# Performance work log

Measured on AMD Instinct MI355X. Metric: run time of the kernel, lower is better.

The kernel has to match this reference:

```python
import jax, jax.numpy as jnp
import numpy as np

N_NODES = 50000
N_EDGES = 600000
IN_DIM = 128
OUT_DIM = 128
N_REL = 32
N_BASES = 4
BN_EPS = 1e-5


def setup_inputs() -> dict:
    key = jax.random.key(0)
    ks = jax.random.split(key, 8)
    entity_emb = jax.random.normal(ks[0], (N_NODES, IN_DIM), dtype=jnp.float32)
    bases = jax.random.normal(ks[1], (N_BASES, IN_DIM, OUT_DIM), dtype=jnp.float32) * 0.05
    coefficients = jax.random.normal(ks[2], (N_REL, N_BASES), dtype=jnp.float32) * 0.5
    W_loop = jax.random.normal(ks[3], (IN_DIM, OUT_DIM), dtype=jnp.float32) * 0.05
    b_loop = jnp.zeros((OUT_DIM,), dtype=jnp.float32)
    gamma = jnp.ones((OUT_DIM,), dtype=jnp.float32)
    beta = jnp.zeros((OUT_DIM,), dtype=jnp.float32)
    edge_index = jax.random.randint(ks[4], (2, N_EDGES), 0, N_NODES, dtype=jnp.int32)
    edge_type = jax.random.randint(ks[5], (N_EDGES,), 0, N_REL, dtype=jnp.int32)
    return {"entity_emb": entity_emb, "bases": bases, "coefficients": coefficients,
            "W_loop": W_loop, "b_loop": b_loop, "gamma": gamma, "beta": beta,
            "edge_index": edge_index, "edge_type": edge_type}


def reference(entity_emb, bases, coefficients, W_loop, b_loop, gamma, beta, edge_index, edge_type):
    N = entity_emb.shape[0]
    # self-loop linear
    out = entity_emb @ W_loop + b_loop  # [N, out_dim]
    # basis decomposition: per-relation weight W[r] = sum_b coeff[r,b] * bases[b]
    W = jnp.einsum('rb,bio->rio', coefficients, bases)  # [R, in, out]
    src, dst = edge_index[0], edge_index[1]
    # per-edge message: entity_emb[src_e] @ W[edge_type_e]  (vectorizes the per-relation loop)
    msg = jnp.einsum('ei,eio->eo', entity_emb[src], W[edge_type])  # [E, out]
    out = out + jax.ops.segment_sum(msg, dst, num_segments=N)
    # degree normalization (in-degree over all edges, clamped at 1)
    deg = jax.ops.segment_sum(jnp.ones_like(dst, dtype=out.dtype), dst, num_segments=N)
    out = out / jnp.maximum(deg, 1.0)[:, None]
    # BatchNorm1d (training mode: biased batch stats over node dim)
    mean = jnp.mean(out, axis=0)
    var = jnp.mean((out - mean) ** 2, axis=0)
    out = (out - mean) / jnp.sqrt(var + BN_EPS) * gamma + beta
    return jax.nn.relu(out)
```

## Files before the change

### kernel.cpp

```cpp
#include <hip/hip_runtime.h>
#include <cstdint>

#define NN 50000
#define NE 600000

typedef unsigned short ushort_t;
typedef __bf16 bf16_t;
typedef __attribute__((ext_vector_type(8))) bf16_t bf16x8;
typedef __attribute__((ext_vector_type(8))) ushort_t ushort8;
typedef __attribute__((ext_vector_type(4))) float f32x4;

#define WT_OFF   0ul
#define XG_OFF   40960ul
#define XBF_OFF  16040960ul
#define CNT_OFF  19240960ul
#define CUR_OFF  19290960ul
#define BSUM_OFF 19340960ul
#define BSCN_OFF 19341088ul
#define CS_OFF   19341216ul
#define CSQ_OFF  19341344ul

__device__ __forceinline__ float2 bf2_to_f2(uint32_t u) {
    float2 r;
    r.x = __uint_as_float(u << 16);
    r.y = __uint_as_float(u & 0xffff0000u);
    return r;
}

__device__ __forceinline__ ushort_t f2bf(float f) {
    uint32_t u = __float_as_uint(f);
    u = (u + 0x7fffu + ((u >> 16) & 1u)) >> 16;
    return (ushort_t)u;
}

__device__ __forceinline__ uint32_t f2bf2(float x, float y) {
    return (uint32_t)f2bf(x) | ((uint32_t)f2bf(y) << 16);
}

__device__ __forceinline__ void async_copy16(const void* g, void* l) {
    __builtin_amdgcn_global_load_lds(
        (const __attribute__((address_space(1))) void*)g,
        (__attribute__((address_space(3))) void*)l, 16, 0, 0);
}

__global__ __launch_bounds__(256) void k_prep(
    const float* __restrict__ Wl, const float* __restrict__ bases,
    ushort_t* __restrict__ WT)
{
    const int i = blockIdx.x * 256 + threadIdx.x;
    if (i >= 128 * 640) return;
    const int n = i / 640;
    const int kk = i - n * 640;
    float v;
    if (kk < 128) v = Wl[kk * 128 + n];
    else {
        const int j = kk - 128;
        v = bases[(size_t)(j >> 7) * 16384 + (j & 127) * 128 + n];
    }
    WT[i] = f2bf(v);
}

__global__ __launch_bounds__(256) void k_cast(
    const float* __restrict__ X, ushort_t* __restrict__ Xbf,
    ushort_t* __restrict__ XG)
{
    __shared__ ushort_t L[16][136];
    const int tid = threadIdx.x;
    const int tile = blockIdx.x;
    {
        const int row = tid >> 4, gc = tid & 15;
        const int node = tile * 16 + row;
        const float4* p = (const float4*)(X + (size_t)node * 128 + gc * 8);
        const float4 a = p[0], b = p[1];
        ushort_t t8[8] = { f2bf(a.x), f2bf(a.y), f2bf(a.z), f2bf(a.w),
                           f2bf(b.x), f2bf(b.y), f2bf(b.z), f2bf(b.w) };
        const uint4 v = *(const uint4*)t8;
        *(uint4*)&L[row][gc * 8] = v;
        *(uint4*)(Xbf + (size_t)node * 128 + gc * 8) = v;
    }
    __syncthreads();
    {
        const int g = tid >> 4, r2 = tid & 15;
        const uint4 u = *(const uint4*)&L[r2][g * 8];
        *(uint4*)(XG + (size_t)tile * 10240 + g * 128 + r2 * 8) = u;
    }
}

__global__ __launch_bounds__(256) void k_hist(
    const int* __restrict__ eidx, int* __restrict__ cnt)
{
    const int* __restrict__ dst = eidx + NE;
    for (int e = blockIdx.x * 256 + threadIdx.x; e < NE; e += gridDim.x * 256)
        atomicAdd(cnt + dst[e], 1);
}

__global__ __launch_bounds__(256) void k_scan1(
    const int* __restrict__ cnt, int* __restrict__ curs, int* __restrict__ bsum)
{
    __shared__ int sh[256];
    const int tid = threadIdx.x;
    const int i0 = blockIdx.x * 512 + tid * 2;
    const int v0 = (i0 < NN) ? cnt[i0] : 0;
    const int v1 = (i0 + 1 < NN) ? cnt[i0 + 1] : 0;
    int s = v0 + v1;
    sh[tid] = s;
    __syncthreads();
#pragma unroll
    for (int off = 1; off < 256; off <<= 1) {
        int t = (tid >= off) ? sh[tid - off] : 0;
        __syncthreads();
        sh[tid] += t;
        __syncthreads();
    }
    const int excl = sh[tid] - s;
    if (i0 < NN) curs[i0] = excl;
    if (i0 + 1 < NN) curs[i0 + 1] = excl + v0;
    if (tid == 255) bsum[blockIdx.x] = sh[255];
}

__global__ __launch_bounds__(128) void k_scan2(
    const int* __restrict__ bsum, int* __restrict__ bscan, int nblk)
{
    __shared__ int sh[128];
    const int tid = threadIdx.x;
    int v = (tid < nblk) ? bsum[tid] : 0;
    sh[tid] = v;
    __syncthreads();
#pragma unroll
    for (int off = 1; off < 128; off <<= 1) {
        int t = (tid >= off) ? sh[tid - off] : 0;
        __syncthreads();
        sh[tid] += t;
        __syncthreads();
    }
    if (tid < nblk) bscan[tid] = sh[tid] - v;
}

__global__ __launch_bounds__(256) void k_scan3(
    int* __restrict__ curs, const int* __restrict__ bscan)
{
    const int add = bscan[blockIdx.x];
    const int i0 = blockIdx.x * 512 + threadIdx.x * 2;
    if (i0 < NN) curs[i0] += add;
    if (i0 + 1 < NN) curs[i0 + 1] += add;
}

__global__ __launch_bounds__(256) void k_scatter(
    const int* __restrict__ eidx, const int* __restrict__ etype,
    int* __restrict__ curs, uint32_t* __restrict__ epack)
{
    const int* __restrict__ src = eidx;
    const int* __restrict__ dst = eidx + NE;
    for (int e = blockIdx.x * 256 + threadIdx.x; e < NE; e += gridDim.x * 256) {
        const int d = dst[e];
        const int pos = atomicAdd(curs + d, 1);
        epack[pos] = (uint32_t)src[e] | ((uint32_t)etype[e] << 16);
    }
}

__device__ __forceinline__ void edge_accum8(
    uint32_t ep, const ushort_t* __restrict__ Xbf,
    const float* __restrict__ coeff, int k, float* m)
{
    const int s = ep & 0xffff;
    const int t = ep >> 16;
    const float4 cw = *(const float4*)(coeff + t * 4);
    const uint4 xv = *(const uint4*)(Xbf + (size_t)s * 128 + k * 8);
    float x[8];
    float2 p;
    p = bf2_to_f2(xv.x); x[0] = p.x; x[1] = p.y;
    p = bf2_to_f2(xv.y); x[2] = p.x; x[3] = p.y;
    p = bf2_to_f2(xv.z); x[4] = p.x; x[5] = p.y;
    p = bf2_to_f2(xv.w); x[6] = p.x; x[7] = p.y;
#pragma unroll
    for (int c = 0; c < 8; ++c) {
        m[0 * 8 + c] += cw.x * x[c];
        m[1 * 8 + c] += cw.y * x[c];
        m[2 * 8 + c] += cw.z * x[c];
        m[3 * 8 + c] += cw.w * x[c];
    }
}

__global__ __launch_bounds__(256) void k_gather(
    const ushort_t* __restrict__ Xbf, const uint32_t* __restrict__ epack,
    const int* __restrict__ cnt, const int* __restrict__ curs,
    const float* __restrict__ coeff, ushort_t* __restrict__ XG)
{
    const int lane = threadIdx.x & 63;
    const int w = threadIdx.x >> 6;
    const int sub = lane >> 4;
    const int k = lane & 15;
    const int tile = blockIdx.x;
    const int d = tile * 16 + w * 4 + sub;

    const int n = cnt[d];
    const int end = curs[d];
    int j = end - n;

    float m[32];
#pragma unroll
    for (int i = 0; i < 32; ++i) m[i] = 0.f;

    for (; j + 3 < end; j += 4) {
        const uint32_t e0 = epack[j];
        const uint32_t e1 = epack[j + 1];
        const uint32_t e2 = epack[j + 2];
        const uint32_t e3 = epack[j + 3];
        edge_accum8(e0, Xbf, coeff, k, m);
        edge_accum8(e1, Xbf, coeff, k, m);
        edge_accum8(e2, Xbf, coeff, k, m);
        edge_accum8(e3, Xbf, coeff, k, m);
    }
    for (; j < end; ++j) edge_accum8(epack[j], Xbf, coeff, k, m);

    uint32_t* gb = (uint32_t*)(XG + (size_t)tile * 10240);
#pragma unroll
    for (int b = 0; b < 4; ++b) {
        uint4 v;
        v.x = f2bf2(m[b * 8 + 0], m[b * 8 + 1]);
        v.y = f2bf2(m[b * 8 + 2], m[b * 8 + 3]);
        v.z = f2bf2(m[b * 8 + 4], m[b * 8 + 5]);
        v.w = f2bf2(m[b * 8 + 6], m[b * 8 + 7]);
        *(uint4*)(gb + (16 + b * 16 + k) * 64 + (w * 4 + sub) * 4) = v;
    }
}

__global__ __launch_bounds__(256) void k_gemm_f(
    const ushort_t* __restrict__ XG, const ushort_t* __restrict__ WT,
    const float* __restrict__ bl, const int* __restrict__ cnt,
    float* __restrict__ out, float* __restrict__ colsum,
    float* __restrict__ colsq)
{
    __shared__ ushort_t As[2][10240];
    const int tid = threadIdx.x;
    const int lane = tid & 63;
    const int w = tid >> 6;
    const int row0 = blockIdx.x * 32;
    const int tile0 = blockIdx.x * 2;

#pragma unroll
    for (int k = 0; k < 10; ++k) {
        const int s = w * 10 + k;
        const int tl = s >= 20 ? 1 : 0;
        const int off = s - tl * 20;
        const ushort_t* src = XG + (size_t)(tile0 + tl) * 10240 + off * 512 + lane * 8;
        async_copy16(src, &As[tl][off * 512]);
    }
    __syncthreads();

    const int m = lane & 15;
    const int quad = lane >> 4;
    const ushort_t* bp0 = WT + (size_t)(w * 32 + m) * 640 + quad * 8;
    const ushort_t* bp1 = bp0 + 16 * 640;

    f32x4 cc[2][2];
#pragma unroll
    for (int rt = 0; rt < 2; ++rt)
#pragma unroll
        for (int ct = 0; ct < 2; ++ct)
#pragma unroll
            for (int i = 0; i < 4; ++i) cc[rt][ct][i] = 0.f;

#pragma unroll
    for (int c = 0; c < 20; ++c) {
        const bf16x8 b0 = __builtin_bit_cast(bf16x8, *(const ushort8*)(bp0 + c * 32));
        const bf16x8 b1 = __builtin_bit_cast(bf16x8, *(const ushort8*)(bp1 + c * 32));
        const int aoff = (c * 4 + quad) * 128 + m * 8;
        const bf16x8 a0 = __builtin_bit_cast(bf16x8, *(const ushort8*)&As[0][aoff]);
        const bf16x8 a1 = __builtin_bit_cast(bf16x8, *(const ushort8*)&As[1][aoff]);
        cc[0][0] = __builtin_amdgcn_mfma_f32_16x16x32_bf16(a0, b0, cc[0][0], 0, 0, 0);
        cc[0][1] = __builtin_amdgcn_mfma_f32_16x16x32_bf16(a0, b1, cc[0][1], 0, 0, 0);
        cc[1][0] = __builtin_amdgcn_mfma_f32_16x16x32_bf16(a1, b0, cc[1][0], 0, 0, 0);
        cc[1][1] = __builtin_amdgcn_mfma_f32_16x16x32_bf16(a1, b1, cc[1][1], 0, 0, 0);
    }

    const float blv0 = bl[w * 32 + m];
    const float blv1 = bl[w * 32 + 16 + m];
    float s0 = 0.f, q0 = 0.f, s1 = 0.f, q1 = 0.f;

#pragma unroll
    for (int rt = 0; rt < 2; ++rt) {
        const int rowb = row0 + rt * 16 + quad * 4;
#pragma unroll
        for (int r = 0; r < 4; ++r) {
            const int row = rowb + r;
            if (row < NN) {
                const int dg = cnt[row];
                const float inv = 1.0f / (float)((dg > 0) ? dg : 1);
                float* po = out + (size_t)row * 128 + w * 32 + m;
                const float v0 = (cc[rt][0][r] + blv0) * inv;
                const float v1 = (cc[rt][1][r] + blv1) * inv;
                po[0]  = v0;
                po[16] = v1;
                s0 += v0; q0 += v0 * v0;
                s1 += v1; q1 += v1 * v1;
            }
        }
    }

    s0 += __shfl_down(s0, 32); q0 += __shfl_down(q0, 32);
    s0 += __shfl_down(s0, 16); q0 += __shfl_down(q0, 16);
    s1 += __shfl_down(s1, 32); q1 += __shfl_down(q1, 32);
    s1 += __shfl_down(s1, 16); q1 += __shfl_down(q1, 16);
    if (lane < 16) {
        atomicAdd(colsum + w * 32 + lane, s0);
        atomicAdd(colsq  + w * 32 + lane, q0);
        atomicAdd(colsum + w * 32 + 16 + lane, s1);
        atomicAdd(colsq  + w * 32 + 16 + lane, q1);
    }
}

__global__ __launch_bounds__(256) void k_bn_relu(
    float* __restrict__ out, const float* __restrict__ colsum,
    const float* __restrict__ colsq, const float* __restrict__ gamma,
    const float* __restrict__ beta)
{
    __shared__ float sc[128], sh[128];
    const int tid = threadIdx.x;
    if (tid < 128) {
        const float mean = colsum[tid] * (1.0f / NN);
        const float var = colsq[tid] * (1.0f / NN) - mean * mean;
        const float g = gamma[tid] * rsqrtf(var + 1e-5f);
        sc[tid] = g;
        sh[tid] = beta[tid] - mean * g;
    }
    __syncthreads();
    const int total = NN * 32;
    for (int i = blockIdx.x * 256 + tid; i < total; i += gridDim.x * 256) {
        const int c = (i & 31) << 2;
        float4 v = *(float4*)(out + (size_t)i * 4);
        v.x = fmaxf(fmaf(v.x, sc[c + 0], sh[c + 0]), 0.f);
        v.y = fmaxf(fmaf(v.y, sc[c + 1], sh[c + 1]), 0.f);
        v.z = fmaxf(fmaf(v.z, sc[c + 2], sh[c + 2]), 0.f);
        v.w = fmaxf(fmaf(v.w, sc[c + 3], sh[c + 3]), 0.f);
        *(float4*)(out + (size_t)i * 4) = v;
    }
}

extern "C" void kernel_launch(void* const* d_in, const int* in_sizes, int n_in,
                              void* d_out, int out_size, void* d_ws, size_t ws_size,
                              hipStream_t stream)
{
    const float* X      = (const float*)d_in[0];
    const float* bases  = (const float*)d_in[1];
    const float* coeff  = (const float*)d_in[2];
    const float* Wl     = (const float*)d_in[3];
    const float* bl     = (const float*)d_in[4];
    const float* gamma  = (const float*)d_in[5];
    const float* beta   = (const float*)d_in[6];
    const int*   eidx   = (const int*)d_in[7];
    const int*   etype  = (const int*)d_in[8];
    float* out = (float*)d_out;

    float* ws = (float*)d_ws;
    ushort_t* WT     = (ushort_t*)(ws + WT_OFF);
    ushort_t* XG     = (ushort_t*)(ws + XG_OFF);
    ushort_t* Xbf    = (ushort_t*)(ws + XBF_OFF);
    int*      cnt    = (int*)(ws + CNT_OFF);
    int*      curs   = (int*)(ws + CUR_OFF);
    int*      bsum   = (int*)(ws + BSUM_OFF);
    int*      bscan  = (int*)(ws + BSCN_OFF);
    float*    colsum = ws + CS_OFF;
    float*    colsq  = ws + CSQ_OFF;
    uint32_t* epack  = (uint32_t*)d_out;

    hipMemsetAsync(cnt, 0, (CSQ_OFF + 128 - CNT_OFF) * sizeof(float), stream);

    const int nblk_scan = (NN + 511) / 512;

    k_prep<<<(128 * 640 + 255) / 256, 256, 0, stream>>>(Wl, bases, WT);
    k_cast<<<3125, 256, 0, stream>>>(X, Xbf, XG);
    k_hist<<<512, 256, 0, stream>>>(eidx, cnt);
    k_scan1<<<nblk_scan, 256, 0, stream>>>(cnt, curs, bsum);
    k_scan2<<<1, 128, 0, stream>>>(bsum, bscan, nblk_scan);
    k_scan3<<<nblk_scan, 256, 0, stream>>>(curs, bscan);
    k_scatter<<<512, 256, 0, stream>>>(eidx, etype, curs, epack);
    k_gather<<<3125, 256, 0, stream>>>(Xbf, epack, cnt, curs, coeff, XG);
    k_gemm_f<<<1563, 256, 0, stream>>>(XG, WT, bl, cnt, out, colsum, colsq);
    k_bn_relu<<<1024, 256, 0, stream>>>(out, colsum, colsq, gamma, beta);
}
```

Measured before the change: 289.2 us.

## Make fused GEMM persistent with double-buffered LDS staging and register-resident weights

The GEMM kernel becomes a grid-stride persistent kernel with 512 blocks. Each block loads its slice of the weight matrix into registers once and double-buffers the async LDS copies of the A tiles, so the next tile's load overlaps the current MFMA work. This also cuts the number of column-stat atomics per block. In exchange it holds 40 ushort8 weight vectors per thread under a 2-blocks-per-CU launch bound, doubles the LDS footprint, and leaves fewer blocks to hide latency.

```diff
diff --git a/kernel.cpp b/kernel.cpp
--- a/kernel.cpp
+++ b/kernel.cpp
@@ -3,6 +3,8 @@
 
 #define NN 50000
 #define NE 600000
+#define NPAIRS 1563
+#define GSTRIDE 512
 
 typedef unsigned short ushort_t;
 typedef __bf16 bf16_t;
@@ -225,77 +227,98 @@
     }
 }
 
-__global__ __launch_bounds__(256) void k_gemm_f(
+__global__ __launch_bounds__(256, 2) void k_gemm_f(
     const ushort_t* __restrict__ XG, const ushort_t* __restrict__ WT,
     const float* __restrict__ bl, const int* __restrict__ cnt,
     float* __restrict__ out, float* __restrict__ colsum,
     float* __restrict__ colsq)
 {
-    __shared__ ushort_t As[2][10240];
+    __shared__ ushort_t As[2][2][10240];
     const int tid = threadIdx.x;
     const int lane = tid & 63;
     const int w = tid >> 6;
-    const int row0 = blockIdx.x * 32;
-    const int tile0 = blockIdx.x * 2;
-
-#pragma unroll
-    for (int k = 0; k < 10; ++k) {
-        const int s = w * 10 + k;
-        const int tl = s >= 20 ? 1 : 0;
-        const int off = s - tl * 20;
-        const ushort_t* src = XG + (size_t)(tile0 + tl) * 10240 + off * 512 + lane * 8;
-        async_copy16(src, &As[tl][off * 512]);
-    }
-    __syncthreads();
-
     const int m = lane & 15;
     const int quad = lane >> 4;
+
+    auto stage = [&](int buf, int pr) {
+        const ushort_t* base = XG + (size_t)pr * 20480;
+#pragma unroll
+        for (int j = 0; j < 10; ++j) {
+            const int idx = w * 10 + j;
+            const int tl = idx / 20;
+            const int off = idx - tl * 20;
+            async_copy16(base + (size_t)tl * 10240 + off * 512 + lane * 8,
+                         &As[buf][tl][off * 512]);
+        }
+    };
+
+    int p = blockIdx.x;
+    stage(0, p);
+
     const ushort_t* bp0 = WT + (size_t)(w * 32 + m) * 640 + quad * 8;
     const ushort_t* bp1 = bp0 + 16 * 640;
-
-    f32x4 cc[2][2];
-#pragma unroll
-    for (int rt = 0; rt < 2; ++rt)
-#pragma unroll
-        for (int ct = 0; ct < 2; ++ct)
-#pragma unroll
-            for (int i = 0; i < 4; ++i) cc[rt][ct][i] = 0.f;
-
+    ushort8 B0[20], B1[20];
 #pragma unroll
     for (int c = 0; c < 20; ++c) {
-        const bf16x8 b0 = __builtin_bit_cast(bf16x8, *(const ushort8*)(bp0 + c * 32));
-        const bf16x8 b1 = __builtin_bit_cast(bf16x8, *(const ushort8*)(bp1 + c * 32));
-        const int aoff = (c * 4 + quad) * 128 + m * 8;
-        const bf16x8 a0 = __builtin_bit_cast(bf16x8, *(const ushort8*)&As[0][aoff]);
-        const bf16x8 a1 = __builtin_bit_cast(bf16x8, *(const ushort8*)&As[1][aoff]);
-        cc[0][0] = __builtin_amdgcn_mfma_f32_16x16x32_bf16(a0, b0, cc[0][0], 0, 0, 0);
-        cc[0][1] = __builtin_amdgcn_mfma_f32_16x16x32_bf16(a0, b1, cc[0][1], 0, 0, 0);
-        cc[1][0] = __builtin_amdgcn_mfma_f32_16x16x32_bf16(a1, b0, cc[1][0], 0, 0, 0);
-        cc[1][1] = __builtin_amdgcn_mfma_f32_16x16x32_bf16(a1, b1, cc[1][1], 0, 0, 0);
-    }
-
+        B0[c] = *(const ushort8*)(bp0 + c * 32);
+        B1[c] = *(const ushort8*)(bp1 + c * 32);
+    }
     const float blv0 = bl[w * 32 + m];
     const float blv1 = bl[w * 32 + 16 + m];
     float s0 = 0.f, q0 = 0.f, s1 = 0.f, q1 = 0.f;
 
-#pragma unroll
-    for (int rt = 0; rt < 2; ++rt) {
-        const int rowb = row0 + rt * 16 + quad * 4;
-#pragma unroll
-        for (int r = 0; r < 4; ++r) {
-            const int row = rowb + r;
-            if (row < NN) {
-                const int dg = cnt[row];
-                const float inv = 1.0f / (float)((dg > 0) ? dg : 1);
-                float* po = out + (size_t)row * 128 + w * 32 + m;
-                const float v0 = (cc[rt][0][r] + blv0) * inv;
-                const float v1 = (cc[rt][1][r] + blv1) * inv;
-                po[0]  = v0;
-                po[16] = v1;
-                s0 += v0; q0 += v0 * v0;
-                s1 += v1; q1 += v1 * v1;
+    __syncthreads();
+
+    int buf = 0;
+    while (p < NPAIRS) {
+        const int pn = p + GSTRIDE;
+        if (pn < NPAIRS) stage(buf ^ 1, pn);
+
+        f32x4 cc[2][2];
+#pragma unroll
+        for (int rt = 0; rt < 2; ++rt)
+#pragma unroll
+            for (int ct = 0; ct < 2; ++ct)
+#pragma unroll
+                for (int i = 0; i < 4; ++i) cc[rt][ct][i] = 0.f;
+
+#pragma unroll
+        for (int c = 0; c < 20; ++c) {
+            const int aoff = (c * 4 + quad) * 128 + m * 8;
+            const bf16x8 a0 = __builtin_bit_cast(bf16x8, *(const ushort8*)&As[buf][0][aoff]);
+            const bf16x8 a1 = __builtin_bit_cast(bf16x8, *(const ushort8*)&As[buf][1][aoff]);
+            const bf16x8 b0 = __builtin_bit_cast(bf16x8, B0[c]);
+            const bf16x8 b1 = __builtin_bit_cast(bf16x8, B1[c]);
+            cc[0][0] = __builtin_amdgcn_mfma_f32_16x16x32_bf16(a0, b0, cc[0][0], 0, 0, 0);
+            cc[0][1] = __builtin_amdgcn_mfma_f32_16x16x32_bf16(a0, b1, cc[0][1], 0, 0, 0);
+            cc[1][0] = __builtin_amdgcn_mfma_f32_16x16x32_bf16(a1, b0, cc[1][0], 0, 0, 0);
+            cc[1][1] = __builtin_amdgcn_mfma_f32_16x16x32_bf16(a1, b1, cc[1][1], 0, 0, 0);
+        }
+
+        const int row0 = p * 32;
+#pragma unroll
+        for (int rt = 0; rt < 2; ++rt) {
+            const int rowb = row0 + rt * 16 + quad * 4;
+#pragma unroll
+            for (int r = 0; r < 4; ++r) {
+                const int row = rowb + r;
+                if (row < NN) {
+                    const int dg = cnt[row];
+                    const float inv = 1.0f / (float)((dg > 0) ? dg : 1);
+                    float* po = out + (size_t)row * 128 + w * 32 + m;
+                    const float v0 = (cc[rt][0][r] + blv0) * inv;
+                    const float v1 = (cc[rt][1][r] + blv1) * inv;
+                    po[0]  = v0;
+                    po[16] = v1;
+                    s0 += v0; q0 += v0 * v0;
+                    s1 += v1; q1 += v1 * v1;
+                }
             }
         }
+
+        if (pn < NPAIRS) __syncthreads();
+        buf ^= 1;
+        p = pn;
     }
 
     s0 += __shfl_down(s0, 32); q0 += __shfl_down(q0, 32);
@@ -376,6 +399,6 @@
     k_scan3<<<nblk_scan, 256, 0, stream>>>(curs, bscan);
     k_scatter<<<512, 256, 0, stream>>>(eidx, etype, curs, epack);
     k_gather<<<3125, 256, 0, stream>>>(Xbf, epack, cnt, curs, coeff, XG);
-    k_gemm_f<<<1563, 256, 0, stream>>>(XG, WT, bl, cnt, out, colsum, colsq);
+    k_gemm_f<<<GSTRIDE, 256, 0, stream>>>(XG, WT, bl, cnt, out, colsum, colsq);
     k_bn_relu<<<1024, 256, 0, stream>>>(out, colsum, colsq, gamma, beta);
 }
```

Result: faster. 262.1 us (-9.4%).
